# Kernel optimization log

Measured on AMD Instinct MI355X. Metric: run time of the kernel, lower is better.

## Reference

```python
import jax, jax.numpy as jnp
import numpy as np

N_QUBITS = 10
N_LATENT = 6
N_LAYERS = 2
AMP_DIM = 2 ** N_QUBITS  # 1024


def _apply_1q(state, gate, q):
    # state: [B] + [2]*N_QUBITS complex; gate: [2,2]; wire q -> axis q+1 (wire 0 = MSB)
    s = jnp.tensordot(gate, state, axes=[[1], [q + 1]])  # new axis at front
    return jnp.moveaxis(s, 0, q + 1)


def _ry_mat(theta):
    c = jnp.cos(theta / 2)
    s = jnp.sin(theta / 2)
    return jnp.stack([jnp.stack([c, -s]), jnp.stack([s, c])]).astype(jnp.complex64)


def _rz_mat(theta):
    half = theta / 2
    e = jnp.cos(half) + 1j * jnp.sin(half)  # e^{i theta/2}
    zero = jnp.zeros((), jnp.complex64)
    return jnp.stack([jnp.stack([jnp.conj(e), zero]), jnp.stack([zero, e])]).astype(jnp.complex64)


def _cnot(state, c, t):
    # flip target axis where control bit == 1
    ctrl_shape = [1] * (N_QUBITS + 1)
    ctrl_shape[c + 1] = 2
    ctrl = jnp.arange(2).reshape(ctrl_shape)
    return jnp.where(ctrl == 1, jnp.flip(state, axis=t + 1), state)


def _expvals(state):
    # PauliX, PauliY, PauliZ on wires 0..N_LATENT-1  -> [B, 3*N_LATENT]
    rest = tuple(range(1, N_QUBITS))  # axes of the 9 remaining wires after a take
    xs, ys, zs = [], [], []
    for q in range(N_LATENT):
        s0 = jnp.take(state, 0, axis=q + 1)
        s1 = jnp.take(state, 1, axis=q + 1)
        z01 = jnp.conj(s0) * s1
        xs.append(2.0 * jnp.sum(z01.real, axis=rest))
        ys.append(2.0 * jnp.sum(z01.imag, axis=rest))
        zs.append(jnp.sum(jnp.abs(s0) ** 2 - jnp.abs(s1) ** 2, axis=rest))
    return jnp.stack(xs + ys + zs, axis=1)


def _simulate(x, weights):
    B, D = x.shape
    if D < AMP_DIM:
        x = jnp.pad(x, ((0, 0), (0, AMP_DIM - D)))
    else:
        x = x[:, :AMP_DIM]
    norm = jnp.maximum(jnp.linalg.norm(x, axis=-1, keepdims=True), 1e-8)
    x = x / norm
    state = x.astype(jnp.complex64).reshape((B,) + (2,) * N_QUBITS)
    for layer in range(N_LAYERS):
        off = layer * N_QUBITS * 3
        for q in range(N_QUBITS):
            state = _apply_1q(state, _ry_mat(weights[off + q]), q)
        for q in range(N_QUBITS):
            state = _apply_1q(state, _rz_mat(weights[off + N_QUBITS + q]), q)
        for q in range(N_QUBITS):
            state = _cnot(state, q, (q + 1) % N_QUBITS)
        for q in range(N_QUBITS):
            state = _apply_1q(state, _ry_mat(weights[off + 2 * N_QUBITS + q]), q)
    return _expvals(state).astype(jnp.float32)


def setup_inputs() -> dict:
    key = jax.random.key(0)
    k1, k2 = jax.random.split(key)
    B, D = 32768, 768
    x = jax.random.normal(k1, (B, D), dtype=jnp.float32)
    std = np.sqrt(2.0 / (N_QUBITS + N_LAYERS)).astype(np.float32)
    weights = jax.random.normal(k2, (N_LAYERS * N_QUBITS * 3,), dtype=jnp.float32) * std
    return {"x": x, "weights": weights}


def reference(x, weights):
    return _simulate(x, weights)
```

## Files before the change

### kernel.cpp

```cpp
#include <hip/hip_runtime.h>

#define DIN 768

typedef float f2 __attribute__((ext_vector_type(2)));
typedef int i2v __attribute__((ext_vector_type(2)));

#if __has_builtin(__builtin_amdgcn_permlane32_swap)
#define HAVE_PL32 1
#endif
#if __has_builtin(__builtin_amdgcn_permlane16_swap)
#define HAVE_PL16 1
#endif

__device__ __forceinline__ int f2i(float v) { return __builtin_bit_cast(int, v); }
__device__ __forceinline__ float i2f(int v) { return __builtin_bit_cast(float, v); }

template<int CTRL>
__device__ __forceinline__ float dppf(float v) {
  const int i = f2i(v);
  return i2f(__builtin_amdgcn_update_dpp(i, i, CTRL, 0xF, 0xF, true));
}
template<int CTRL>
__device__ __forceinline__ f2 dppf2(f2 v) {
  f2 r; r.x = dppf<CTRL>(v.x); r.y = dppf<CTRL>(v.y); return r;
}

__device__ __forceinline__ f2 wsum2(f2 v) {
  v += dppf2<0xB1>(v);
  v += dppf2<0x4E>(v);
  v += dppf2<0x124>(v);
  v += dppf2<0x128>(v);
#ifdef HAVE_PL16
  { i2v rx = __builtin_amdgcn_permlane16_swap(f2i(v.x), f2i(v.x), false, false);
    i2v ry = __builtin_amdgcn_permlane16_swap(f2i(v.y), f2i(v.y), false, false);
    v.x = i2f(rx.x) + i2f(rx.y);
    v.y = i2f(ry.x) + i2f(ry.y); }
#else
  v.x += __shfl_xor(v.x, 16); v.y += __shfl_xor(v.y, 16);
#endif
#ifdef HAVE_PL32
  { i2v rx = __builtin_amdgcn_permlane32_swap(f2i(v.x), f2i(v.x), false, false);
    i2v ry = __builtin_amdgcn_permlane32_swap(f2i(v.y), f2i(v.y), false, false);
    v.x = i2f(rx.x) + i2f(rx.y);
    v.y = i2f(ry.x) + i2f(ry.y); }
#else
  v.x += __shfl_xor(v.x, 32); v.y += __shfl_xor(v.y, 32);
#endif
  return v;
}

template<int MASK>
__device__ __forceinline__ f2 shflx_f2(f2 v, int lane) {
  f2 r;
  if constexpr (MASK == 1) {
    r = dppf2<0xB1>(v);
  } else if constexpr (MASK == 2) {
    r = dppf2<0x4E>(v);
  } else if constexpr (MASK == 16) {
#ifdef HAVE_PL16
    const i2v a = __builtin_amdgcn_permlane16_swap(f2i(v.x), f2i(v.x), false, false);
    const i2v b = __builtin_amdgcn_permlane16_swap(f2i(v.y), f2i(v.y), false, false);
    const bool hi = (lane >> 4) & 1;
    r.x = hi ? i2f(a.x) : i2f(a.y);
    r.y = hi ? i2f(b.x) : i2f(b.y);
#else
    r.x = __shfl_xor(v.x, 16); r.y = __shfl_xor(v.y, 16);
#endif
  } else if constexpr (MASK == 32) {
#ifdef HAVE_PL32
    const i2v a = __builtin_amdgcn_permlane32_swap(f2i(v.x), f2i(v.x), false, false);
    const i2v b = __builtin_amdgcn_permlane32_swap(f2i(v.y), f2i(v.y), false, false);
    const bool lo = lane < 32;
    r.x = lo ? i2f(a.y) : i2f(a.x);
    r.y = lo ? i2f(b.y) : i2f(b.x);
#else
    r.x = __shfl_xor(v.x, 32); r.y = __shfl_xor(v.y, 32);
#endif
  } else {
    r.x = __shfl_xor(v.x, MASK); r.y = __shfl_xor(v.y, MASK);
  }
  return r;
}

__device__ __forceinline__ int swzf(int i) { return i ^ ((i >> 4) & 31); }

__device__ __forceinline__ int cnotL(int i) {
  const int b9 = (i >> 9) & 1;
  const int b8 = (i >> 8) & 1;
  const int b0 = i & 1;
  return ((i ^ (i >> 1)) & 0xFF) | ((b8 ^ b9 ^ b0) << 8) | ((b9 ^ b0) << 9);
}

template<int RB>
__device__ __forceinline__ void ry1(f2 (&a)[16], float c, float s) {
#pragma unroll
  for (int r = 0; r < 16; ++r) {
    if (!(r & (1 << RB))) {
      const int p = r | (1 << RB);
      const f2 a0 = a[r], a1 = a[p];
      a[r] = a0 * c - a1 * s;
      a[p] = a1 * c + a0 * s;
    }
  }
}
template<int RB>
__device__ __forceinline__ void ry2(f2 (&re)[16], f2 (&im)[16], float c, float s) {
  ry1<RB>(re, c, s);
  ry1<RB>(im, c, s);
}
template<int MASK>
__device__ __forceinline__ void ry1_shfl(int lane, f2 (&a)[16], float c, float s) {
  const float ss = (lane & MASK) ? s : -s;
#pragma unroll
  for (int r = 0; r < 16; ++r) {
    const f2 p = shflx_f2<MASK>(a[r], lane);
    a[r] = a[r] * c + p * ss;
  }
}

template<int RB>
__device__ __forceinline__ void xyr(const f2 (&re)[16], const f2 (&im)[16], f2& aX, f2& aY) {
#pragma unroll
  for (int r = 0; r < 16; ++r) {
    if (!(r & (1 << RB))) {
      const int p = r | (1 << RB);
      aX += re[r] * re[p] + im[r] * im[p];
      aY += re[r] * im[p] - im[r] * re[p];
    }
  }
}
template<int MASK>
__device__ __forceinline__ void xys(int lane, const f2 (&re)[16], const f2 (&im)[16], f2& aX, f2& aY) {
  const float sgn = (lane & MASK) ? -1.f : 1.f;
#pragma unroll
  for (int r = 0; r < 16; ++r) {
    const f2 pr = shflx_f2<MASK>(re[r], lane);
    const f2 pi = shflx_f2<MASK>(im[r], lane);
    aX += re[r] * pr + im[r] * pi;
    aY += (re[r] * pi - im[r] * pr) * sgn;
  }
}

__global__ void qae_prep(const float* __restrict__ w, float2* __restrict__ ws) {
  const int i = threadIdx.x;
  if (i < 50) {
    float s, c; __sincosf(0.5f * w[i], &s, &c);
    ws[i] = make_float2(c, s);
  } else if (i < 56) {
    float s, c; __sincosf(w[i], &s, &c);
    ws[i] = make_float2(c, s);
  } else if (i < 60) {
    ws[i] = make_float2(1.f, 0.f);
  } else if (i < 70) {
    const int q = i - 60;
    float s, c; __sincosf(0.5f * (w[20 + q] + w[30 + q]), &s, &c);
    ws[i] = make_float2(c, s);
  }
  float p1 = 0.f, p2 = 0.f;
#pragma unroll
  for (int b = 0; b < 10; ++b) {
    const float sg = ((i >> b) & 1) ? 0.5f : -0.5f;
    p1 += sg * w[10 + 9 - b];
    p2 += sg * w[40 + 9 - b];
  }
  float s, c;
  __sincosf(p1, &s, &c); ws[70 + i]        = make_float2(c, s);
  __sincosf(p2, &s, &c); ws[70 + 1024 + i] = make_float2(c, s);
}

#define STC(boff) (*reinterpret_cast<f2*>(reinterpret_cast<char*>(stc) + (boff)))

__global__ __launch_bounds__(64) void qae_main(const float* __restrict__ x,
                                               const float2* __restrict__ gt,
                                               float* __restrict__ out, int Btot) {
  __shared__ f2 stc[1024];
  const int lane = threadIdx.x;
  const int b0   = blockIdx.x * 2, b1 = b0 + 1;
  const bool has1 = (b1 < Btot);
  const float2* rz1 = gt + 70;
  const float2* rz2 = gt + 70 + 1024;

  const int bA8  = swzf(lane << 4) << 3;
  const int sL8  = swzf(lane) << 3;
  const int bCA8 = swzf(cnotL(lane << 4)) << 3;
  const int bCB8 = swzf(cnotL(lane)) << 3;

  f2 g[16];
  f2 ss = (f2){0.f, 0.f};
  const float* x0 = x + (size_t)b0 * DIN;
  const float* x1 = x + (size_t)b1 * DIN;
#pragma unroll
  for (int t = 0; t < 4; ++t) {
    const int idx = lane * 16 + 4 * t;
    float4 va = make_float4(0.f, 0.f, 0.f, 0.f);
    float4 vb = make_float4(0.f, 0.f, 0.f, 0.f);
    if (idx < DIN) {
      va = *reinterpret_cast<const float4*>(x0 + idx);
      if (has1) vb = *reinterpret_cast<const float4*>(x1 + idx);
    }
    g[4*t+0] = (f2){va.x, vb.x}; g[4*t+1] = (f2){va.y, vb.y};
    g[4*t+2] = (f2){va.z, vb.z}; g[4*t+3] = (f2){va.w, vb.w};
#pragma unroll
    for (int k = 0; k < 4; ++k) ss += g[4*t+k] * g[4*t+k];
  }
  ss = wsum2(ss);
  const f2 inv = (f2){1.f / fmaxf(ss.x, 1e-16f), 1.f / fmaxf(ss.y, 1e-16f)};

  float2 cs;
  cs = gt[6]; ry1<3>(g, cs.x, cs.y);
  cs = gt[7]; ry1<2>(g, cs.x, cs.y);
  cs = gt[8]; ry1<1>(g, cs.x, cs.y);
  cs = gt[9]; ry1<0>(g, cs.x, cs.y);
  cs = gt[4]; ry1_shfl<2>(lane, g, cs.x, cs.y);
  cs = gt[5]; ry1_shfl<1>(lane, g, cs.x, cs.y);

#pragma unroll
  for (int r = 0; r < 16; ++r) STC(bA8 ^ (r << 3)) = g[r];
#pragma unroll
  for (int r = 0; r < 16; ++r) g[r] = STC((swzf(r << 6) << 3) ^ sL8);

  cs = gt[0]; ry1<3>(g, cs.x, cs.y);
  cs = gt[1]; ry1<2>(g, cs.x, cs.y);
  cs = gt[2]; ry1<1>(g, cs.x, cs.y);
  cs = gt[3]; ry1<0>(g, cs.x, cs.y);

  f2 re[16], im[16];
#pragma unroll
  for (int r = 0; r < 16; ++r) {
    const float2 t = rz1[(r << 6) | lane];
    re[r] = g[r] * t.x;
    im[r] = g[r] * t.y;
  }

#pragma unroll
  for (int r = 0; r < 16; ++r) STC((swzf(r << 6) << 3) ^ sL8) = re[r];
#pragma unroll
  for (int r = 0; r < 16; ++r) re[r] = STC(bCA8 ^ (swzf(cnotL(r)) << 3));
#pragma unroll
  for (int r = 0; r < 16; ++r) STC((swzf(r << 6) << 3) ^ sL8) = im[r];
#pragma unroll
  for (int r = 0; r < 16; ++r) im[r] = STC(bCA8 ^ (swzf(cnotL(r)) << 3));

  cs = gt[66]; ry2<3>(re, im, cs.x, cs.y);
  cs = gt[67]; ry2<2>(re, im, cs.x, cs.y);
  cs = gt[68]; ry2<1>(re, im, cs.x, cs.y);
  cs = gt[69]; ry2<0>(re, im, cs.x, cs.y);
  cs = gt[64]; ry1_shfl<2>(lane, re, cs.x, cs.y); ry1_shfl<2>(lane, im, cs.x, cs.y);
  cs = gt[65]; ry1_shfl<1>(lane, re, cs.x, cs.y); ry1_shfl<1>(lane, im, cs.x, cs.y);

#pragma unroll
  for (int r = 0; r < 16; ++r) STC(bA8 ^ (r << 3)) = re[r];
#pragma unroll
  for (int r = 0; r < 16; ++r) re[r] = STC((swzf(r << 6) << 3) ^ sL8);
#pragma unroll
  for (int r = 0; r < 16; ++r) STC(bA8 ^ (r << 3)) = im[r];
#pragma unroll
  for (int r = 0; r < 16; ++r) im[r] = STC((swzf(r << 6) << 3) ^ sL8);

  cs = gt[60]; ry2<3>(re, im, cs.x, cs.y);
  cs = gt[61]; ry2<2>(re, im, cs.x, cs.y);
  cs = gt[62]; ry2<1>(re, im, cs.x, cs.y);
  cs = gt[63]; ry2<0>(re, im, cs.x, cs.y);

#pragma unroll
  for (int r = 0; r < 16; ++r) {
    const float2 t = rz2[(r << 6) | lane];
    const f2 nre = re[r] * t.x - im[r] * t.y;
    im[r] = re[r] * t.y + im[r] * t.x;
    re[r] = nre;
  }

#pragma unroll
  for (int r = 0; r < 16; ++r) STC((swzf(r << 6) << 3) ^ sL8) = re[r];
#pragma unroll
  for (int r = 0; r < 16; ++r) re[r] = STC(bCB8 ^ (swzf(cnotL(r << 6)) << 3));
#pragma unroll
  for (int r = 0; r < 16; ++r) STC((swzf(r << 6) << 3) ^ sL8) = im[r];
#pragma unroll
  for (int r = 0; r < 16; ++r) im[r] = STC(bCB8 ^ (swzf(cnotL(r << 6)) << 3));

  f2 a18[18];
#pragma unroll
  for (int k = 0; k < 12; ++k) a18[k] = (f2){0.f, 0.f};

  {
    f2 psum = (f2){0.f, 0.f};
    f2 z0 = (f2){0.f,0.f}, z1 = (f2){0.f,0.f}, z2 = (f2){0.f,0.f}, z3 = (f2){0.f,0.f};
#pragma unroll
    for (int r = 0; r < 16; ++r) {
      const f2 p = re[r] * re[r] + im[r] * im[r];
      psum += p;
      z0 += (r & 8) ? -p : p;
      z1 += (r & 4) ? -p : p;
      z2 += (r & 2) ? -p : p;
      z3 += (r & 1) ? -p : p;
    }
    a18[12] = z0; a18[13] = z1; a18[14] = z2; a18[15] = z3;
    a18[16] = ((lane >> 5) & 1) ? -psum : psum;
    a18[17] = ((lane >> 4) & 1) ? -psum : psum;
  }

  xyr<3>(re, im, a18[0], a18[6]);
  xyr<2>(re, im, a18[1], a18[7]);
  xyr<1>(re, im, a18[2], a18[8]);
  xyr<0>(re, im, a18[3], a18[9]);
  xys<32>(lane, re, im, a18[4], a18[10]);
  xys<16>(lane, re, im, a18[5], a18[11]);

#pragma unroll
  for (int k = 0; k < 18; ++k) {
    f2 v = a18[k];
    v += dppf2<0xB1>(v);
    v += dppf2<0x4E>(v);
    a18[k] = v;
  }
  float* red = reinterpret_cast<float*>(stc);
  if ((lane & 3) == 0) {
    const int q = lane >> 2;
    f2* redf2 = reinterpret_cast<f2*>(red);
#pragma unroll
    for (int k = 0; k < 18; ++k) redf2[q * 20 + k] = a18[k];
  }
  if (lane < 36) {
    const int c  = (lane >= 18) ? 1 : 0;
    const int j  = lane - 18 * c;
    const int jq = (j < 6) ? j : ((j < 12) ? j - 6 : j - 12);
    const int jp = (j < 6) ? (j + 12) : ((j >= 12) ? (j - 12) : j);
    float S = 0.f, P = 0.f;
#pragma unroll
    for (int q = 0; q < 16; ++q) {
      S += red[(q * 20 + j ) * 2 + c];
      P += red[(q * 20 + jp) * 2 + c];
    }
    const float fac  = (jq < 4) ? 2.f : 1.f;
    const float2 fa  = gt[50 + jq];
    const float invc = c ? inv.y : inv.x;
    float o;
    if (j < 6)       o = (fac * S * fa.x + P * fa.y) * invc;
    else if (j < 12) o = fac * S * invc;
    else             o = (S * fa.x - fac * P * fa.y) * invc;
    if (c == 0 || has1) out[(size_t)(b0 + c) * 18 + j] = o;
  }
}

extern "C" void kernel_launch(void* const* d_in, const int* in_sizes, int n_in,
                              void* d_out, int out_size, void* d_ws, size_t ws_size,
                              hipStream_t stream) {
  const float* x = (const float*)d_in[0];
  const float* w = (const float*)d_in[1];
  float* out = (float*)d_out;
  float2* ws = (float2*)d_ws;
  const int B = in_sizes[0] / DIN;
  qae_prep<<<dim3(1), dim3(1024), 0, stream>>>(w, ws);
  const int grid = (B + 1) / 2;
  qae_main<<<dim3(grid), dim3(64), 0, stream>>>(x, (const float2*)ws, out, B);
}
```

Baseline: 100.1 us.

## Pack re/im into 16-byte LDS transposes and loop two sample pairs per block

Complex amplitudes are now stored as interleaved re/im float4 in shared memory, so each transpose is a single 16-byte store/load pass instead of two 8-byte passes. Each 64-thread block also processes two pairs of samples sequentially, halving the grid and amortizing setup such as address swizzle computation. The shared buffer doubles to 16 KB, which may limit occupancy. The sequential loop also reduces the parallelism available to hide memory latency.

```diff
diff --git a/kernel.cpp b/kernel.cpp
--- a/kernel.cpp
+++ b/kernel.cpp
@@ -3,6 +3,7 @@
 #define DIN 768
 
 typedef float f2 __attribute__((ext_vector_type(2)));
+typedef float f4 __attribute__((ext_vector_type(4)));
 typedef int i2v __attribute__((ext_vector_type(2)));
 
 #if __has_builtin(__builtin_amdgcn_permlane32_swap)
@@ -168,178 +169,190 @@
   __sincosf(p2, &s, &c); ws[70 + 1024 + i] = make_float2(c, s);
 }
 
-#define STC(boff) (*reinterpret_cast<f2*>(reinterpret_cast<char*>(stc) + (boff)))
+#define STC8(boff)  (*reinterpret_cast<f2*>(reinterpret_cast<char*>(stc) + (boff)))
+#define STC16(boff) (*reinterpret_cast<f4*>(reinterpret_cast<char*>(stc) + (boff)))
 
 __global__ __launch_bounds__(64) void qae_main(const float* __restrict__ x,
                                                const float2* __restrict__ gt,
                                                float* __restrict__ out, int Btot) {
-  __shared__ f2 stc[1024];
+  __shared__ f4 stc[1024];
   const int lane = threadIdx.x;
-  const int b0   = blockIdx.x * 2, b1 = b0 + 1;
-  const bool has1 = (b1 < Btot);
   const float2* rz1 = gt + 70;
   const float2* rz2 = gt + 70 + 1024;
 
-  const int bA8  = swzf(lane << 4) << 3;
-  const int sL8  = swzf(lane) << 3;
-  const int bCA8 = swzf(cnotL(lane << 4)) << 3;
-  const int bCB8 = swzf(cnotL(lane)) << 3;
-
-  f2 g[16];
-  f2 ss = (f2){0.f, 0.f};
-  const float* x0 = x + (size_t)b0 * DIN;
-  const float* x1 = x + (size_t)b1 * DIN;
-#pragma unroll
-  for (int t = 0; t < 4; ++t) {
-    const int idx = lane * 16 + 4 * t;
-    float4 va = make_float4(0.f, 0.f, 0.f, 0.f);
-    float4 vb = make_float4(0.f, 0.f, 0.f, 0.f);
-    if (idx < DIN) {
-      va = *reinterpret_cast<const float4*>(x0 + idx);
-      if (has1) vb = *reinterpret_cast<const float4*>(x1 + idx);
-    }
-    g[4*t+0] = (f2){va.x, vb.x}; g[4*t+1] = (f2){va.y, vb.y};
-    g[4*t+2] = (f2){va.z, vb.z}; g[4*t+3] = (f2){va.w, vb.w};
-#pragma unroll
-    for (int k = 0; k < 4; ++k) ss += g[4*t+k] * g[4*t+k];
-  }
-  ss = wsum2(ss);
-  const f2 inv = (f2){1.f / fmaxf(ss.x, 1e-16f), 1.f / fmaxf(ss.y, 1e-16f)};
-
-  float2 cs;
-  cs = gt[6]; ry1<3>(g, cs.x, cs.y);
-  cs = gt[7]; ry1<2>(g, cs.x, cs.y);
-  cs = gt[8]; ry1<1>(g, cs.x, cs.y);
-  cs = gt[9]; ry1<0>(g, cs.x, cs.y);
-  cs = gt[4]; ry1_shfl<2>(lane, g, cs.x, cs.y);
-  cs = gt[5]; ry1_shfl<1>(lane, g, cs.x, cs.y);
-
-#pragma unroll
-  for (int r = 0; r < 16; ++r) STC(bA8 ^ (r << 3)) = g[r];
-#pragma unroll
-  for (int r = 0; r < 16; ++r) g[r] = STC((swzf(r << 6) << 3) ^ sL8);
-
-  cs = gt[0]; ry1<3>(g, cs.x, cs.y);
-  cs = gt[1]; ry1<2>(g, cs.x, cs.y);
-  cs = gt[2]; ry1<1>(g, cs.x, cs.y);
-  cs = gt[3]; ry1<0>(g, cs.x, cs.y);
-
-  f2 re[16], im[16];
-#pragma unroll
-  for (int r = 0; r < 16; ++r) {
-    const float2 t = rz1[(r << 6) | lane];
-    re[r] = g[r] * t.x;
-    im[r] = g[r] * t.y;
-  }
-
-#pragma unroll
-  for (int r = 0; r < 16; ++r) STC((swzf(r << 6) << 3) ^ sL8) = re[r];
-#pragma unroll
-  for (int r = 0; r < 16; ++r) re[r] = STC(bCA8 ^ (swzf(cnotL(r)) << 3));
-#pragma unroll
-  for (int r = 0; r < 16; ++r) STC((swzf(r << 6) << 3) ^ sL8) = im[r];
-#pragma unroll
-  for (int r = 0; r < 16; ++r) im[r] = STC(bCA8 ^ (swzf(cnotL(r)) << 3));
-
-  cs = gt[66]; ry2<3>(re, im, cs.x, cs.y);
-  cs = gt[67]; ry2<2>(re, im, cs.x, cs.y);
-  cs = gt[68]; ry2<1>(re, im, cs.x, cs.y);
-  cs = gt[69]; ry2<0>(re, im, cs.x, cs.y);
-  cs = gt[64]; ry1_shfl<2>(lane, re, cs.x, cs.y); ry1_shfl<2>(lane, im, cs.x, cs.y);
-  cs = gt[65]; ry1_shfl<1>(lane, re, cs.x, cs.y); ry1_shfl<1>(lane, im, cs.x, cs.y);
-
-#pragma unroll
-  for (int r = 0; r < 16; ++r) STC(bA8 ^ (r << 3)) = re[r];
-#pragma unroll
-  for (int r = 0; r < 16; ++r) re[r] = STC((swzf(r << 6) << 3) ^ sL8);
-#pragma unroll
-  for (int r = 0; r < 16; ++r) STC(bA8 ^ (r << 3)) = im[r];
-#pragma unroll
-  for (int r = 0; r < 16; ++r) im[r] = STC((swzf(r << 6) << 3) ^ sL8);
-
-  cs = gt[60]; ry2<3>(re, im, cs.x, cs.y);
-  cs = gt[61]; ry2<2>(re, im, cs.x, cs.y);
-  cs = gt[62]; ry2<1>(re, im, cs.x, cs.y);
-  cs = gt[63]; ry2<0>(re, im, cs.x, cs.y);
-
-#pragma unroll
-  for (int r = 0; r < 16; ++r) {
-    const float2 t = rz2[(r << 6) | lane];
-    const f2 nre = re[r] * t.x - im[r] * t.y;
-    im[r] = re[r] * t.y + im[r] * t.x;
-    re[r] = nre;
-  }
-
-#pragma unroll
-  for (int r = 0; r < 16; ++r) STC((swzf(r << 6) << 3) ^ sL8) = re[r];
-#pragma unroll
-  for (int r = 0; r < 16; ++r) re[r] = STC(bCB8 ^ (swzf(cnotL(r << 6)) << 3));
-#pragma unroll
-  for (int r = 0; r < 16; ++r) STC((swzf(r << 6) << 3) ^ sL8) = im[r];
-#pragma unroll
-  for (int r = 0; r < 16; ++r) im[r] = STC(bCB8 ^ (swzf(cnotL(r << 6)) << 3));
-
-  f2 a18[18];
-#pragma unroll
-  for (int k = 0; k < 12; ++k) a18[k] = (f2){0.f, 0.f};
-
-  {
-    f2 psum = (f2){0.f, 0.f};
-    f2 z0 = (f2){0.f,0.f}, z1 = (f2){0.f,0.f}, z2 = (f2){0.f,0.f}, z3 = (f2){0.f,0.f};
-#pragma unroll
-    for (int r = 0; r < 16; ++r) {
-      const f2 p = re[r] * re[r] + im[r] * im[r];
-      psum += p;
-      z0 += (r & 8) ? -p : p;
-      z1 += (r & 4) ? -p : p;
-      z2 += (r & 2) ? -p : p;
-      z3 += (r & 1) ? -p : p;
-    }
-    a18[12] = z0; a18[13] = z1; a18[14] = z2; a18[15] = z3;
-    a18[16] = ((lane >> 5) & 1) ? -psum : psum;
-    a18[17] = ((lane >> 4) & 1) ? -psum : psum;
-  }
-
-  xyr<3>(re, im, a18[0], a18[6]);
-  xyr<2>(re, im, a18[1], a18[7]);
-  xyr<1>(re, im, a18[2], a18[8]);
-  xyr<0>(re, im, a18[3], a18[9]);
-  xys<32>(lane, re, im, a18[4], a18[10]);
-  xys<16>(lane, re, im, a18[5], a18[11]);
-
-#pragma unroll
-  for (int k = 0; k < 18; ++k) {
-    f2 v = a18[k];
-    v += dppf2<0xB1>(v);
-    v += dppf2<0x4E>(v);
-    a18[k] = v;
-  }
-  float* red = reinterpret_cast<float*>(stc);
-  if ((lane & 3) == 0) {
-    const int q = lane >> 2;
-    f2* redf2 = reinterpret_cast<f2*>(red);
-#pragma unroll
-    for (int k = 0; k < 18; ++k) redf2[q * 20 + k] = a18[k];
-  }
-  if (lane < 36) {
-    const int c  = (lane >= 18) ? 1 : 0;
-    const int j  = lane - 18 * c;
-    const int jq = (j < 6) ? j : ((j < 12) ? j - 6 : j - 12);
-    const int jp = (j < 6) ? (j + 12) : ((j >= 12) ? (j - 12) : j);
-    float S = 0.f, P = 0.f;
-#pragma unroll
-    for (int q = 0; q < 16; ++q) {
-      S += red[(q * 20 + j ) * 2 + c];
-      P += red[(q * 20 + jp) * 2 + c];
-    }
-    const float fac  = (jq < 4) ? 2.f : 1.f;
-    const float2 fa  = gt[50 + jq];
-    const float invc = c ? inv.y : inv.x;
-    float o;
-    if (j < 6)       o = (fac * S * fa.x + P * fa.y) * invc;
-    else if (j < 12) o = fac * S * invc;
-    else             o = (S * fa.x - fac * P * fa.y) * invc;
-    if (c == 0 || has1) out[(size_t)(b0 + c) * 18 + j] = o;
+  const int bA8   = swzf(lane << 4) << 3;
+  const int sL8   = swzf(lane) << 3;
+  const int bA16  = swzf(lane << 4) << 4;
+  const int sL16  = swzf(lane) << 4;
+  const int bCA16 = swzf(cnotL(lane << 4)) << 4;
+  const int bCB16 = swzf(cnotL(lane)) << 4;
+
+#pragma unroll 1
+  for (int bp = 0; bp < 2; ++bp) {
+    const int b0 = blockIdx.x * 4 + bp * 2;
+    if (b0 >= Btot) break;
+    const int b1 = b0 + 1;
+    const bool has1 = (b1 < Btot);
+
+    f2 g[16];
+    f2 ss = (f2){0.f, 0.f};
+    const float* x0 = x + (size_t)b0 * DIN;
+    const float* x1 = x + (size_t)b1 * DIN;
+#pragma unroll
+    for (int t = 0; t < 4; ++t) {
+      const int idx = lane * 16 + 4 * t;
+      float4 va = make_float4(0.f, 0.f, 0.f, 0.f);
+      float4 vb = make_float4(0.f, 0.f, 0.f, 0.f);
+      if (idx < DIN) {
+        va = *reinterpret_cast<const float4*>(x0 + idx);
+        if (has1) vb = *reinterpret_cast<const float4*>(x1 + idx);
+      }
+      g[4*t+0] = (f2){va.x, vb.x}; g[4*t+1] = (f2){va.y, vb.y};
+      g[4*t+2] = (f2){va.z, vb.z}; g[4*t+3] = (f2){va.w, vb.w};
+#pragma unroll
+      for (int k = 0; k < 4; ++k) ss += g[4*t+k] * g[4*t+k];
+    }
+    ss = wsum2(ss);
+    const f2 inv = (f2){1.f / fmaxf(ss.x, 1e-16f), 1.f / fmaxf(ss.y, 1e-16f)};
+
+    float2 cs;
+    cs = gt[6]; ry1<3>(g, cs.x, cs.y);
+    cs = gt[7]; ry1<2>(g, cs.x, cs.y);
+    cs = gt[8]; ry1<1>(g, cs.x, cs.y);
+    cs = gt[9]; ry1<0>(g, cs.x, cs.y);
+    cs = gt[4]; ry1_shfl<2>(lane, g, cs.x, cs.y);
+    cs = gt[5]; ry1_shfl<1>(lane, g, cs.x, cs.y);
+
+#pragma unroll
+    for (int r = 0; r < 16; ++r) STC8(bA8 ^ (r << 3)) = g[r];
+#pragma unroll
+    for (int r = 0; r < 16; ++r) g[r] = STC8((swzf(r << 6) << 3) ^ sL8);
+
+    cs = gt[0]; ry1<3>(g, cs.x, cs.y);
+    cs = gt[1]; ry1<2>(g, cs.x, cs.y);
+    cs = gt[2]; ry1<1>(g, cs.x, cs.y);
+    cs = gt[3]; ry1<0>(g, cs.x, cs.y);
+
+    f2 re[16], im[16];
+#pragma unroll
+    for (int r = 0; r < 16; ++r) {
+      const float2 t = rz1[(r << 6) | lane];
+      re[r] = g[r] * t.x;
+      im[r] = g[r] * t.y;
+    }
+
+#pragma unroll
+    for (int r = 0; r < 16; ++r)
+      STC16(sL16 ^ (swzf(r << 6) << 4)) = __builtin_shufflevector(re[r], im[r], 0, 1, 2, 3);
+#pragma unroll
+    for (int r = 0; r < 16; ++r) {
+      const f4 v = STC16(bCA16 ^ (swzf(cnotL(r)) << 4));
+      re[r] = __builtin_shufflevector(v, v, 0, 1);
+      im[r] = __builtin_shufflevector(v, v, 2, 3);
+    }
+
+    cs = gt[66]; ry2<3>(re, im, cs.x, cs.y);
+    cs = gt[67]; ry2<2>(re, im, cs.x, cs.y);
+    cs = gt[68]; ry2<1>(re, im, cs.x, cs.y);
+    cs = gt[69]; ry2<0>(re, im, cs.x, cs.y);
+    cs = gt[64]; ry1_shfl<2>(lane, re, cs.x, cs.y); ry1_shfl<2>(lane, im, cs.x, cs.y);
+    cs = gt[65]; ry1_shfl<1>(lane, re, cs.x, cs.y); ry1_shfl<1>(lane, im, cs.x, cs.y);
+
+#pragma unroll
+    for (int r = 0; r < 16; ++r)
+      STC16(bA16 ^ (r << 4)) = __builtin_shufflevector(re[r], im[r], 0, 1, 2, 3);
+#pragma unroll
+    for (int r = 0; r < 16; ++r) {
+      const f4 v = STC16((swzf(r << 6) << 4) ^ sL16);
+      re[r] = __builtin_shufflevector(v, v, 0, 1);
+      im[r] = __builtin_shufflevector(v, v, 2, 3);
+    }
+
+    cs = gt[60]; ry2<3>(re, im, cs.x, cs.y);
+    cs = gt[61]; ry2<2>(re, im, cs.x, cs.y);
+    cs = gt[62]; ry2<1>(re, im, cs.x, cs.y);
+    cs = gt[63]; ry2<0>(re, im, cs.x, cs.y);
+
+#pragma unroll
+    for (int r = 0; r < 16; ++r) {
+      const float2 t = rz2[(r << 6) | lane];
+      const f2 nre = re[r] * t.x - im[r] * t.y;
+      im[r] = re[r] * t.y + im[r] * t.x;
+      re[r] = nre;
+    }
+
+#pragma unroll
+    for (int r = 0; r < 16; ++r)
+      STC16(sL16 ^ (swzf(r << 6) << 4)) = __builtin_shufflevector(re[r], im[r], 0, 1, 2, 3);
+#pragma unroll
+    for (int r = 0; r < 16; ++r) {
+      const f4 v = STC16(bCB16 ^ (swzf(cnotL(r << 6)) << 4));
+      re[r] = __builtin_shufflevector(v, v, 0, 1);
+      im[r] = __builtin_shufflevector(v, v, 2, 3);
+    }
+
+    f2 a18[18];
+#pragma unroll
+    for (int k = 0; k < 12; ++k) a18[k] = (f2){0.f, 0.f};
+
+    {
+      f2 psum = (f2){0.f, 0.f};
+      f2 z0 = (f2){0.f,0.f}, z1 = (f2){0.f,0.f}, z2 = (f2){0.f,0.f}, z3 = (f2){0.f,0.f};
+#pragma unroll
+      for (int r = 0; r < 16; ++r) {
+        const f2 p = re[r] * re[r] + im[r] * im[r];
+        psum += p;
+        z0 += (r & 8) ? -p : p;
+        z1 += (r & 4) ? -p : p;
+        z2 += (r & 2) ? -p : p;
+        z3 += (r & 1) ? -p : p;
+      }
+      a18[12] = z0; a18[13] = z1; a18[14] = z2; a18[15] = z3;
+      a18[16] = ((lane >> 5) & 1) ? -psum : psum;
+      a18[17] = ((lane >> 4) & 1) ? -psum : psum;
+    }
+
+    xyr<3>(re, im, a18[0], a18[6]);
+    xyr<2>(re, im, a18[1], a18[7]);
+    xyr<1>(re, im, a18[2], a18[8]);
+    xyr<0>(re, im, a18[3], a18[9]);
+    xys<32>(lane, re, im, a18[4], a18[10]);
+    xys<16>(lane, re, im, a18[5], a18[11]);
+
+#pragma unroll
+    for (int k = 0; k < 18; ++k) {
+      f2 v = a18[k];
+      v += dppf2<0xB1>(v);
+      v += dppf2<0x4E>(v);
+      a18[k] = v;
+    }
+    float* red = reinterpret_cast<float*>(stc);
+    if ((lane & 3) == 0) {
+      const int q = lane >> 2;
+      f2* redf2 = reinterpret_cast<f2*>(red);
+#pragma unroll
+      for (int k = 0; k < 18; ++k) redf2[q * 20 + k] = a18[k];
+    }
+    if (lane < 36) {
+      const int c  = (lane >= 18) ? 1 : 0;
+      const int j  = lane - 18 * c;
+      const int jq = (j < 6) ? j : ((j < 12) ? j - 6 : j - 12);
+      const int jp = (j < 6) ? (j + 12) : ((j >= 12) ? (j - 12) : j);
+      float S = 0.f, P = 0.f;
+#pragma unroll
+      for (int q = 0; q < 16; ++q) {
+        S += red[(q * 20 + j ) * 2 + c];
+        P += red[(q * 20 + jp) * 2 + c];
+      }
+      const float fac  = (jq < 4) ? 2.f : 1.f;
+      const float2 fa  = gt[50 + jq];
+      const float invc = c ? inv.y : inv.x;
+      float o;
+      if (j < 6)       o = (fac * S * fa.x + P * fa.y) * invc;
+      else if (j < 12) o = fac * S * invc;
+      else             o = (S * fa.x - fac * P * fa.y) * invc;
+      if (c == 0 || has1) out[(size_t)(b0 + c) * 18 + j] = o;
+    }
   }
 }
 
@@ -352,6 +365,6 @@
   float2* ws = (float2*)d_ws;
   const int B = in_sizes[0] / DIN;
   qae_prep<<<dim3(1), dim3(1024), 0, stream>>>(w, ws);
-  const int grid = (B + 1) / 2;
+  const int grid = (B + 3) / 4;
   qae_main<<<dim3(grid), dim3(64), 0, stream>>>(x, (const float2*)ws, out, B);
 }
```

Measured after the change: 150.4 us. 50.3% more time.

## Load input in row-major lane layout, drop first LDS transpose, factor RZ phase tables

Applied to the files above, without the earlier changes.

Input is now loaded with amplitude index (r<<6)|lane, so the first RY layer runs directly in the register-row layout. Lane-dimension rotations use DPP, ds_swizzle and permlane cross-lane exchanges, which removes one shared-memory store/load transpose. The 1024-entry RZ phase tables are factored into a 16-entry row table and a 64-entry lane table that are multiplied at runtime, which shrinks global table reads. The cost is more cross-lane shuffles and scalar loads instead of coalesced float4 loads.

```diff
diff --git a/kernel.cpp b/kernel.cpp
--- a/kernel.cpp
+++ b/kernel.cpp
@@ -56,6 +56,11 @@
     r = dppf2<0xB1>(v);
   } else if constexpr (MASK == 2) {
     r = dppf2<0x4E>(v);
+  } else if constexpr (MASK == 4) {
+    r.x = i2f(__builtin_amdgcn_ds_swizzle(f2i(v.x), 0x101F));
+    r.y = i2f(__builtin_amdgcn_ds_swizzle(f2i(v.y), 0x101F));
+  } else if constexpr (MASK == 8) {
+    r = dppf2<0x128>(v);
   } else if constexpr (MASK == 16) {
 #ifdef HAVE_PL16
     const i2v a = __builtin_amdgcn_permlane16_swap(f2i(v.x), f2i(v.x), false, false);
@@ -156,19 +161,33 @@
     float s, c; __sincosf(0.5f * (w[20 + q] + w[30 + q]), &s, &c);
     ws[i] = make_float2(c, s);
   }
-  float p1 = 0.f, p2 = 0.f;
-#pragma unroll
-  for (int b = 0; b < 10; ++b) {
-    const float sg = ((i >> b) & 1) ? 0.5f : -0.5f;
-    p1 += sg * w[10 + 9 - b];
-    p2 += sg * w[40 + 9 - b];
-  }
-  float s, c;
-  __sincosf(p1, &s, &c); ws[70 + i]        = make_float2(c, s);
-  __sincosf(p2, &s, &c); ws[70 + 1024 + i] = make_float2(c, s);
-}
-
-#define STC(boff) (*reinterpret_cast<f2*>(reinterpret_cast<char*>(stc) + (boff)))
+  if (i < 16) {
+    float p1 = 0.f, p2 = 0.f;
+#pragma unroll
+    for (int k = 0; k < 4; ++k) {
+      const float sg = ((i >> k) & 1) ? 0.5f : -0.5f;
+      p1 += sg * w[10 + 3 - k];
+      p2 += sg * w[40 + 3 - k];
+    }
+    float s, c;
+    __sincosf(p1, &s, &c); ws[70 + i] = make_float2(c, s);
+    __sincosf(p2, &s, &c); ws[86 + i] = make_float2(c, s);
+  }
+  if (i < 64) {
+    float p1 = 0.f, p2 = 0.f;
+#pragma unroll
+    for (int b = 0; b < 6; ++b) {
+      const float sg = ((i >> b) & 1) ? 0.5f : -0.5f;
+      p1 += sg * w[10 + 9 - b];
+      p2 += sg * w[40 + 9 - b];
+    }
+    float s, c;
+    __sincosf(p1, &s, &c); ws[102 + i] = make_float2(c, s);
+    __sincosf(p2, &s, &c); ws[166 + i] = make_float2(c, s);
+  }
+}
+
+#define STC8(boff) (*reinterpret_cast<f2*>(reinterpret_cast<char*>(stc) + (boff)))
 
 __global__ __launch_bounds__(64) void qae_main(const float* __restrict__ x,
                                                const float2* __restrict__ gt,
@@ -177,69 +196,62 @@
   const int lane = threadIdx.x;
   const int b0   = blockIdx.x * 2, b1 = b0 + 1;
   const bool has1 = (b1 < Btot);
-  const float2* rz1 = gt + 70;
-  const float2* rz2 = gt + 70 + 1024;
-
-  const int bA8  = swzf(lane << 4) << 3;
-  const int sL8  = swzf(lane) << 3;
-  const int bCA8 = swzf(cnotL(lane << 4)) << 3;
-  const int bCB8 = swzf(cnotL(lane)) << 3;
+
+  const float2 L1 = gt[102 + lane];
+  const float2 L2 = gt[166 + lane];
+
+  const int bA8   = swzf(lane << 4) << 3;
+  const int sL8   = swzf(lane) << 3;
+  const int bCA8  = swzf(cnotL(lane << 4)) << 3;
+  const int bCB8  = swzf(cnotL(lane)) << 3;
 
   f2 g[16];
   f2 ss = (f2){0.f, 0.f};
   const float* x0 = x + (size_t)b0 * DIN;
   const float* x1 = x + (size_t)b1 * DIN;
 #pragma unroll
-  for (int t = 0; t < 4; ++t) {
-    const int idx = lane * 16 + 4 * t;
-    float4 va = make_float4(0.f, 0.f, 0.f, 0.f);
-    float4 vb = make_float4(0.f, 0.f, 0.f, 0.f);
-    if (idx < DIN) {
-      va = *reinterpret_cast<const float4*>(x0 + idx);
-      if (has1) vb = *reinterpret_cast<const float4*>(x1 + idx);
-    }
-    g[4*t+0] = (f2){va.x, vb.x}; g[4*t+1] = (f2){va.y, vb.y};
-    g[4*t+2] = (f2){va.z, vb.z}; g[4*t+3] = (f2){va.w, vb.w};
-#pragma unroll
-    for (int k = 0; k < 4; ++k) ss += g[4*t+k] * g[4*t+k];
-  }
+  for (int r = 0; r < 12; ++r) {
+    const int i = (r << 6) | lane;
+    const float va = x0[i];
+    const float vb = has1 ? x1[i] : 0.f;
+    g[r] = (f2){va, vb};
+    ss += g[r] * g[r];
+  }
+#pragma unroll
+  for (int r = 12; r < 16; ++r) g[r] = (f2){0.f, 0.f};
   ss = wsum2(ss);
   const f2 inv = (f2){1.f / fmaxf(ss.x, 1e-16f), 1.f / fmaxf(ss.y, 1e-16f)};
 
   float2 cs;
-  cs = gt[6]; ry1<3>(g, cs.x, cs.y);
-  cs = gt[7]; ry1<2>(g, cs.x, cs.y);
-  cs = gt[8]; ry1<1>(g, cs.x, cs.y);
-  cs = gt[9]; ry1<0>(g, cs.x, cs.y);
-  cs = gt[4]; ry1_shfl<2>(lane, g, cs.x, cs.y);
-  cs = gt[5]; ry1_shfl<1>(lane, g, cs.x, cs.y);
-
-#pragma unroll
-  for (int r = 0; r < 16; ++r) STC(bA8 ^ (r << 3)) = g[r];
-#pragma unroll
-  for (int r = 0; r < 16; ++r) g[r] = STC((swzf(r << 6) << 3) ^ sL8);
-
   cs = gt[0]; ry1<3>(g, cs.x, cs.y);
   cs = gt[1]; ry1<2>(g, cs.x, cs.y);
   cs = gt[2]; ry1<1>(g, cs.x, cs.y);
   cs = gt[3]; ry1<0>(g, cs.x, cs.y);
+  cs = gt[4]; ry1_shfl<32>(lane, g, cs.x, cs.y);
+  cs = gt[5]; ry1_shfl<16>(lane, g, cs.x, cs.y);
+  cs = gt[6]; ry1_shfl<8>(lane, g, cs.x, cs.y);
+  cs = gt[7]; ry1_shfl<4>(lane, g, cs.x, cs.y);
+  cs = gt[8]; ry1_shfl<2>(lane, g, cs.x, cs.y);
+  cs = gt[9]; ry1_shfl<1>(lane, g, cs.x, cs.y);
 
   f2 re[16], im[16];
 #pragma unroll
   for (int r = 0; r < 16; ++r) {
-    const float2 t = rz1[(r << 6) | lane];
-    re[r] = g[r] * t.x;
-    im[r] = g[r] * t.y;
-  }
-
-#pragma unroll
-  for (int r = 0; r < 16; ++r) STC((swzf(r << 6) << 3) ^ sL8) = re[r];
-#pragma unroll
-  for (int r = 0; r < 16; ++r) re[r] = STC(bCA8 ^ (swzf(cnotL(r)) << 3));
-#pragma unroll
-  for (int r = 0; r < 16; ++r) STC((swzf(r << 6) << 3) ^ sL8) = im[r];
-#pragma unroll
-  for (int r = 0; r < 16; ++r) im[r] = STC(bCA8 ^ (swzf(cnotL(r)) << 3));
+    const float2 R = gt[70 + r];
+    const float kre = R.x * L1.x - R.y * L1.y;
+    const float kim = R.x * L1.y + R.y * L1.x;
+    re[r] = g[r] * kre;
+    im[r] = g[r] * kim;
+  }
+
+#pragma unroll
+  for (int r = 0; r < 16; ++r) STC8((swzf(r << 6) << 3) ^ sL8) = re[r];
+#pragma unroll
+  for (int r = 0; r < 16; ++r) re[r] = STC8(bCA8 ^ (swzf(cnotL(r)) << 3));
+#pragma unroll
+  for (int r = 0; r < 16; ++r) STC8((swzf(r << 6) << 3) ^ sL8) = im[r];
+#pragma unroll
+  for (int r = 0; r < 16; ++r) im[r] = STC8(bCA8 ^ (swzf(cnotL(r)) << 3));
 
   cs = gt[66]; ry2<3>(re, im, cs.x, cs.y);
   cs = gt[67]; ry2<2>(re, im, cs.x, cs.y);
@@ -249,13 +261,13 @@
   cs = gt[65]; ry1_shfl<1>(lane, re, cs.x, cs.y); ry1_shfl<1>(lane, im, cs.x, cs.y);
 
 #pragma unroll
-  for (int r = 0; r < 16; ++r) STC(bA8 ^ (r << 3)) = re[r];
-#pragma unroll
-  for (int r = 0; r < 16; ++r) re[r] = STC((swzf(r << 6) << 3) ^ sL8);
-#pragma unroll
-  for (int r = 0; r < 16; ++r) STC(bA8 ^ (r << 3)) = im[r];
-#pragma unroll
-  for (int r = 0; r < 16; ++r) im[r] = STC((swzf(r << 6) << 3) ^ sL8);
+  for (int r = 0; r < 16; ++r) STC8(bA8 ^ (r << 3)) = re[r];
+#pragma unroll
+  for (int r = 0; r < 16; ++r) re[r] = STC8((swzf(r << 6) << 3) ^ sL8);
+#pragma unroll
+  for (int r = 0; r < 16; ++r) STC8(bA8 ^ (r << 3)) = im[r];
+#pragma unroll
+  for (int r = 0; r < 16; ++r) im[r] = STC8((swzf(r << 6) << 3) ^ sL8);
 
   cs = gt[60]; ry2<3>(re, im, cs.x, cs.y);
   cs = gt[61]; ry2<2>(re, im, cs.x, cs.y);
@@ -264,20 +276,22 @@
 
 #pragma unroll
   for (int r = 0; r < 16; ++r) {
-    const float2 t = rz2[(r << 6) | lane];
-    const f2 nre = re[r] * t.x - im[r] * t.y;
-    im[r] = re[r] * t.y + im[r] * t.x;
+    const float2 R = gt[86 + r];
+    const float kre = R.x * L2.x - R.y * L2.y;
+    const float kim = R.x * L2.y + R.y * L2.x;
+    const f2 nre = re[r] * kre - im[r] * kim;
+    im[r] = re[r] * kim + im[r] * kre;
     re[r] = nre;
   }
 
 #pragma unroll
-  for (int r = 0; r < 16; ++r) STC((swzf(r << 6) << 3) ^ sL8) = re[r];
-#pragma unroll
-  for (int r = 0; r < 16; ++r) re[r] = STC(bCB8 ^ (swzf(cnotL(r << 6)) << 3));
-#pragma unroll
-  for (int r = 0; r < 16; ++r) STC((swzf(r << 6) << 3) ^ sL8) = im[r];
-#pragma unroll
-  for (int r = 0; r < 16; ++r) im[r] = STC(bCB8 ^ (swzf(cnotL(r << 6)) << 3));
+  for (int r = 0; r < 16; ++r) STC8((swzf(r << 6) << 3) ^ sL8) = re[r];
+#pragma unroll
+  for (int r = 0; r < 16; ++r) re[r] = STC8(bCB8 ^ (swzf(cnotL(r << 6)) << 3));
+#pragma unroll
+  for (int r = 0; r < 16; ++r) STC8((swzf(r << 6) << 3) ^ sL8) = im[r];
+#pragma unroll
+  for (int r = 0; r < 16; ++r) im[r] = STC8(bCB8 ^ (swzf(cnotL(r << 6)) << 3));
 
   f2 a18[18];
 #pragma unroll
```

After: 102.9 us. 2.8% more time.
